# Kernel optimization log

Measured on AMD Instinct MI355X. Metric: run time of the kernel, lower is better.

## Reference

```python
import jax, jax.numpy as jnp
import numpy as np

N_Q, M, D, DV = 4096, 32768, 512, 512  # groups, keys, key dim, value dim


def setup_inputs() -> dict:
    key = jax.random.key(0)
    k1, k2, k3 = jax.random.split(key, 3)
    query = jax.random.normal(k1, (N_Q, D), dtype=jnp.float32)
    keys = jax.random.normal(k2, (M, D), dtype=jnp.float32)
    values = jax.random.normal(k3, (M, DV), dtype=jnp.float32)
    # each query/group owns exactly M//N_Q keys -> no empty softmax rows
    tree_idx = jnp.arange(M, dtype=jnp.int32) % N_Q
    return {"query": query, "keys": keys, "values": values, "tree_idx": tree_idx}


def _l2_normalize(x, eps=1e-12):
    # matches F.normalize(x, dim=1, p=2): x / max(||x||_2, eps)
    n = jnp.linalg.norm(x, axis=1, keepdims=True)
    return x / jnp.maximum(n, eps)


def reference(query, keys, values, tree_idx):
    n_q = query.shape[0]
    # mask[q, m] = (tree_idx[m] == q); equivalent to zeros.index_add(0, tree_idx, eye(M)).bool()
    mask = tree_idx[None, :] == jnp.arange(n_q, dtype=tree_idx.dtype)[:, None]  # [N_q, M]
    query_n = _l2_normalize(query)
    keys_n = _l2_normalize(keys)
    align = query_n @ keys_n.T                      # [N_q, M] cosine similarities
    align = jnp.where(mask, align, -jnp.inf)        # masked_fill_(~mask, -inf)
    alpha = jax.nn.softmax(align, axis=1)           # segment-masked softmax per query
    att = alpha @ values                            # [N_q, DV]
    return att, alpha.sum(axis=0)
```

## Files before the change

kernel.cpp:

```cpp
#include <hip/hip_runtime.h>
#include <math.h>

#define D_DIM 512

__device__ __forceinline__ float d4(const float4& a, const float4& b) {
    return a.x*b.x + a.y*b.y + a.z*b.z + a.w*b.w;
}
__device__ __forceinline__ void fma4(float4& a, float w, const float4& v) {
    a.x += w*v.x; a.y += w*v.y; a.z += w*v.z; a.w += w*v.w;
}

__global__ void k_fill(const int* __restrict__ tree_idx, int m_total, int n_q,
                       int cap, int* __restrict__ cnt, int* __restrict__ keyslot) {
    const int i = blockIdx.x * blockDim.x + threadIdx.x;
    const int base = cnt[n_q];
    if (i < m_total) {
        const int q = tree_idx[i];
        const int old = atomicAdd(&cnt[q], 1);
        const int slot = (int)((unsigned)old - (unsigned)base);
        if (slot >= 0 && slot < cap) keyslot[(size_t)q * cap + slot] = i;
    }
}

__global__ __launch_bounds__(256, 8) void attn_main(
        const float* __restrict__ query, const float* __restrict__ keys,
        const float* __restrict__ values, const int* __restrict__ cnt,
        const int* __restrict__ keyslot, int cap,
        const int* __restrict__ tree_idx, int m_total,
        float* __restrict__ att, float* __restrict__ colsum, int n_q) {
    __shared__ float4 s_acc[2][128];
    __shared__ float  s_ps[2][2];
    const int lane = threadIdx.x & 63;
    const int wv   = threadIdx.x >> 6;
    const int ql   = wv >> 1;
    const int h    = wv & 1;
    const int qi   = (blockIdx.x << 1) + ql;
    const bool act = qi < n_q;

    float e0 = 0.f, e1 = 0.f, e2 = 0.f, e3 = 0.f;
    int   m0 = 0, m1 = 0, m2 = 0, m3 = 0;
    bool  ok0 = false, ok1 = false, ok2 = false, ok3 = false;
    float4 aa = make_float4(0.f, 0.f, 0.f, 0.f);
    float4 ab = make_float4(0.f, 0.f, 0.f, 0.f);
    size_t off = 0;
    int nk = 0;
    bool fast = false;

    if (act) {
        const int base = cnt[n_q];
        nk = (int)((unsigned)cnt[qi] - (unsigned)base);
        if (nk < 0) nk = 0;
        if (nk > cap) nk = cap;
        off  = (size_t)qi * cap;
        fast = (nk == 8);
        const float4* qp = (const float4*)(query + (size_t)qi * D_DIM);
        float4 qa = qp[lane], qb = qp[lane + 64];
        float pq = d4(qa, qa) + d4(qb, qb);
        float psum = 0.f;

        if (fast) {
            m0 = keyslot[off + h];     m1 = keyslot[off + h + 2];
            m2 = keyslot[off + h + 4]; m3 = keyslot[off + h + 6];
            ok0 = (m0 >= 0 && m0 < m_total && tree_idx[m0] == qi);
            ok1 = (m1 >= 0 && m1 < m_total && tree_idx[m1] == qi);
            ok2 = (m2 >= 0 && m2 < m_total && tree_idx[m2] == qi);
            ok3 = (m3 >= 0 && m3 < m_total && tree_idx[m3] == qi);
            int c0 = ok0 ? m0 : 0, c1 = ok1 ? m1 : 0;
            int c2 = ok2 ? m2 : 0, c3 = ok3 ? m3 : 0;
            const float4* k0 = (const float4*)(keys + (size_t)c0 * D_DIM);
            const float4* k1 = (const float4*)(keys + (size_t)c1 * D_DIM);
            const float4* k2 = (const float4*)(keys + (size_t)c2 * D_DIM);
            const float4* k3 = (const float4*)(keys + (size_t)c3 * D_DIM);
            float4 x0a = k0[lane], x0b = k0[lane + 64];
            float4 x1a = k1[lane], x1b = k1[lane + 64];
            float pd0 = d4(qa, x0a) + d4(qb, x0b), pk0 = d4(x0a, x0a) + d4(x0b, x0b);
            float pd1 = d4(qa, x1a) + d4(qb, x1b), pk1 = d4(x1a, x1a) + d4(x1b, x1b);
            float4 x2a = k2[lane], x2b = k2[lane + 64];
            float4 x3a = k3[lane], x3b = k3[lane + 64];
            float pd2 = d4(qa, x2a) + d4(qb, x2b), pk2 = d4(x2a, x2a) + d4(x2b, x2b);
            float pd3 = d4(qa, x3a) + d4(qb, x3b), pk3 = d4(x3a, x3a) + d4(x3b, x3b);
#pragma unroll
            for (int o = 32; o > 0; o >>= 1) {
                pq  += __shfl_xor(pq,  o);
                pd0 += __shfl_xor(pd0, o); pk0 += __shfl_xor(pk0, o);
                pd1 += __shfl_xor(pd1, o); pk1 += __shfl_xor(pk1, o);
                pd2 += __shfl_xor(pd2, o); pk2 += __shfl_xor(pk2, o);
                pd3 += __shfl_xor(pd3, o); pk3 += __shfl_xor(pk3, o);
            }
            const float qinv = 1.0f / fmaxf(sqrtf(pq), 1e-12f);
            e0 = ok0 ? __expf(pd0 * qinv / fmaxf(sqrtf(pk0), 1e-12f)) : 0.f;
            e1 = ok1 ? __expf(pd1 * qinv / fmaxf(sqrtf(pk1), 1e-12f)) : 0.f;
            e2 = ok2 ? __expf(pd2 * qinv / fmaxf(sqrtf(pk2), 1e-12f)) : 0.f;
            e3 = ok3 ? __expf(pd3 * qinv / fmaxf(sqrtf(pk3), 1e-12f)) : 0.f;
            psum = e0 + e1 + e2 + e3;
            if (lane == 0) s_ps[ql][h] = psum;
            const float4* v0 = (const float4*)(values + (size_t)c0 * D_DIM);
            const float4* v1 = (const float4*)(values + (size_t)c1 * D_DIM);
            const float4* v2 = (const float4*)(values + (size_t)c2 * D_DIM);
            const float4* v3 = (const float4*)(values + (size_t)c3 * D_DIM);
            float4 y0a = v0[lane], y0b = v0[lane + 64];
            float4 y1a = v1[lane], y1b = v1[lane + 64];
            fma4(aa, e0, y0a); fma4(ab, e0, y0b);
            fma4(aa, e1, y1a); fma4(ab, e1, y1b);
            float4 y2a = v2[lane], y2b = v2[lane + 64];
            float4 y3a = v3[lane], y3b = v3[lane + 64];
            fma4(aa, e2, y2a); fma4(ab, e2, y2b);
            fma4(aa, e3, y3a); fma4(ab, e3, y3b);
        } else {
#pragma unroll
            for (int o = 32; o > 0; o >>= 1) pq += __shfl_xor(pq, o);
            const float qinv = 1.0f / fmaxf(sqrtf(pq), 1e-12f);
            for (int j = h; j < nk; j += 2) {
                int mi = keyslot[off + j];
                bool ok = (mi >= 0 && mi < m_total && tree_idx[mi] == qi);
                int ci = ok ? mi : 0;
                const float4* kp = (const float4*)(keys   + (size_t)ci * D_DIM);
                const float4* vp = (const float4*)(values + (size_t)ci * D_DIM);
                float4 ka = kp[lane], kb = kp[lane + 64];
                float pd = d4(qa, ka) + d4(qb, kb);
                float pk = d4(ka, ka) + d4(kb, kb);
#pragma unroll
                for (int o = 32; o > 0; o >>= 1) {
                    pd += __shfl_xor(pd, o);
                    pk += __shfl_xor(pk, o);
                }
                float e = ok ? __expf(pd * qinv / fmaxf(sqrtf(pk), 1e-12f)) : 0.f;
                psum += e;
                if (lane == 0 && ok) colsum[mi] = e;
                float4 va = vp[lane], vb = vp[lane + 64];
                fma4(aa, e, va); fma4(ab, e, vb);
            }
            if (lane == 0) s_ps[ql][h] = psum;
        }
        if (h == 0) { s_acc[ql][lane] = aa; s_acc[ql][64 + lane] = ab; }
    }
    __syncthreads();
    if (act) {
        const float tot = s_ps[ql][0] + s_ps[ql][1];
        const float inv = (tot > 0.f) ? 1.0f / tot : 0.f;
        if (h == 1) {
            float4 oa = s_acc[ql][lane], ob = s_acc[ql][64 + lane];
            oa.x = (oa.x + aa.x) * inv; oa.y = (oa.y + aa.y) * inv;
            oa.z = (oa.z + aa.z) * inv; oa.w = (oa.w + aa.w) * inv;
            ob.x = (ob.x + ab.x) * inv; ob.y = (ob.y + ab.y) * inv;
            ob.z = (ob.z + ab.z) * inv; ob.w = (ob.w + ab.w) * inv;
            float4* op = (float4*)(att + (size_t)qi * D_DIM);
            op[lane]      = oa;
            op[lane + 64] = ob;
        }
        if (fast) {
            if (lane == 0) {
                if (ok0) colsum[m0] = e0 * inv;
                if (ok1) colsum[m1] = e1 * inv;
                if (ok2) colsum[m2] = e2 * inv;
                if (ok3) colsum[m3] = e3 * inv;
            }
        } else if (lane == 0) {
            for (int j = h; j < nk; j += 2) {
                int mi = keyslot[off + j];
                if (mi >= 0 && mi < m_total && tree_idx[mi] == qi) colsum[mi] *= inv;
            }
        }
    }
}

__global__ void k_zero(int* cnt, int n) {
    int i = blockIdx.x * blockDim.x + threadIdx.x;
    if (i < n) cnt[i] = 0;
}
__global__ void k_count(const int* __restrict__ t, int* __restrict__ cnt, int m) {
    int i = blockIdx.x * blockDim.x + threadIdx.x;
    if (i < m) atomicAdd(&cnt[t[i]], 1);
}
__global__ __launch_bounds__(1024) void k_scan(int* __restrict__ cnt,
                                               int* __restrict__ offsets, int n_q) {
    __shared__ int wsum[16];
    const int tid = threadIdx.x, lane = tid & 63, wv = tid >> 6;
    const int items = (n_q + 1023) >> 10;
    const int base = tid * items;
    int local = 0;
    for (int i = 0; i < items; ++i) { int idx = base + i; if (idx < n_q) local += cnt[idx]; }
    int incl = local;
#pragma unroll
    for (int o = 1; o < 64; o <<= 1) { int v = __shfl_up(incl, o); if (lane >= o) incl += v; }
    if (lane == 63) wsum[wv] = incl;
    __syncthreads();
    if (wv == 0) {
        int v = (lane < 16) ? wsum[lane] : 0;
        int iv = v;
#pragma unroll
        for (int o = 1; o < 16; o <<= 1) { int t = __shfl_up(iv, o); if (lane >= o) iv += t; }
        if (lane < 16) wsum[lane] = iv - v;
    }
    __syncthreads();
    int run = wsum[wv] + incl - local;
    for (int i = 0; i < items; ++i) {
        int idx = base + i;
        if (idx < n_q) { int c = cnt[idx]; offsets[idx] = run; cnt[idx] = run; run += c; }
    }
    if (tid == 1023) offsets[n_q] = run;
}
__global__ void k_scatter(const int* __restrict__ t, int* __restrict__ cnt,
                          int* __restrict__ keylist, int m) {
    int i = blockIdx.x * blockDim.x + threadIdx.x;
    if (i < m) { int p = atomicAdd(&cnt[t[i]], 1); keylist[p] = i; }
}
__global__ __launch_bounds__(512, 8) void attn_fb(
        const float* __restrict__ query, const float* __restrict__ keys,
        const float* __restrict__ values, const int* __restrict__ offsets,
        const int* __restrict__ keylist, float* __restrict__ att,
        float* __restrict__ colsum) {
    __shared__ float4 s_v[8][128];
    __shared__ float  s_e[8];
    const int qi = blockIdx.x, tid = threadIdx.x, lane = tid & 63, wv = tid >> 6;
    const int off = offsets[qi];
    const int nk  = offsets[qi + 1] - off;
    const float4* qp = (const float4*)(query + (size_t)qi * D_DIM);
    float4 qa = qp[lane], qb = qp[lane + 64];
    float pq = d4(qa, qa) + d4(qb, qb);
    float4 aa = make_float4(0,0,0,0), ab = make_float4(0,0,0,0);
    float esum = 0.f;
    for (int idx = wv; idx < nk; idx += 8) {
        const int mi = keylist[off + idx];
        const float4* kp = (const float4*)(keys   + (size_t)mi * D_DIM);
        const float4* vp = (const float4*)(values + (size_t)mi * D_DIM);
        float4 ka = kp[lane], kb = kp[lane + 64];
        float4 va = vp[lane], vb = vp[lane + 64];
        float pd = d4(qa, ka) + d4(qb, kb);
        float pk = d4(ka, ka) + d4(kb, kb);
        float pq2 = pq;
#pragma unroll
        for (int o = 32; o > 0; o >>= 1) {
            pd += __shfl_xor(pd, o); pk += __shfl_xor(pk, o); pq2 += __shfl_xor(pq2, o);
        }
        const float qinv = 1.0f / fmaxf(sqrtf(pq2), 1e-12f);
        const float e = __expf(pd * qinv / fmaxf(sqrtf(pk), 1e-12f));
        esum += e;
        if (lane == 0) colsum[mi] = e;
        fma4(aa, e, va); fma4(ab, e, vb);
    }
    if (lane == 0) s_e[wv] = esum;
    s_v[wv][lane] = aa; s_v[wv][64 + lane] = ab;
    __syncthreads();
    const float tot = s_e[0]+s_e[1]+s_e[2]+s_e[3]+s_e[4]+s_e[5]+s_e[6]+s_e[7];
    const float inv = (tot > 0.f) ? 1.0f / tot : 0.f;
    if (tid < 128) {
        float4 r = s_v[0][tid];
#pragma unroll
        for (int j = 1; j < 8; ++j) { float4 p = s_v[j][tid]; r.x+=p.x; r.y+=p.y; r.z+=p.z; r.w+=p.w; }
        r.x *= inv; r.y *= inv; r.z *= inv; r.w *= inv;
        ((float4*)(att + (size_t)qi * D_DIM))[tid] = r;
    }
    if (lane == 0)
        for (int idx = wv; idx < nk; idx += 8) colsum[keylist[off + idx]] *= inv;
}

extern "C" void kernel_launch(void* const* d_in, const int* in_sizes, int n_in,
                              void* d_out, int out_size, void* d_ws, size_t ws_size,
                              hipStream_t stream) {
    const float* query    = (const float*)d_in[0];
    const float* keys     = (const float*)d_in[1];
    const float* values   = (const float*)d_in[2];
    const int*   tree_idx = (const int*)d_in[3];

    const int n_q     = in_sizes[0] / D_DIM;
    const int m_total = in_sizes[3];

    float* att    = (float*)d_out;
    float* colsum = att + (size_t)n_q * D_DIM;

    const long ws_ints = (long)(ws_size / 4);
    long cap_l = (ws_ints - (n_q + 1)) / (n_q > 0 ? n_q : 1);
    if (cap_l > 1024) cap_l = 1024;

    if (cap_l >= 8) {
        const int cap = (int)cap_l;
        int* cnt     = (int*)d_ws;
        int* keyslot = cnt + n_q + 1;
        k_fill<<<(m_total + 255) / 256, 256, 0, stream>>>(tree_idx, m_total, n_q,
                                                          cap, cnt, keyslot);
        attn_main<<<(n_q + 1) / 2, 256, 0, stream>>>(query, keys, values, cnt,
                                                     keyslot, cap, tree_idx, m_total,
                                                     att, colsum, n_q);
    } else {
        int* cnt     = (int*)d_ws;
        int* offsets = cnt + n_q;
        int* keylist = offsets + n_q + 1;
        k_zero   <<<(n_q + 255) / 256, 256, 0, stream>>>(cnt, n_q);
        k_count  <<<(m_total + 255) / 256, 256, 0, stream>>>(tree_idx, cnt, m_total);
        k_scan   <<<1, 1024, 0, stream>>>(cnt, offsets, n_q);
        k_scatter<<<(m_total + 255) / 256, 256, 0, stream>>>(tree_idx, cnt, keylist, m_total);
        attn_fb  <<<n_q, 512, 0, stream>>>(query, keys, values, offsets, keylist, att, colsum);
    }
}
```

Before: 167.7 us.

## Stage gathered key/value rows into LDS via global_load_lds, one wave per query

Replaces the 4-wave, 2-queries-per-block kernel with a single-wave kernel that processes several queries in sequence. For groups of exactly eight keys, it copies all key and value rows straight into LDS with async global_load_lds before computing, then reads them back from LDS. The goal is more memory-level parallelism for the gathered loads and no cross-wave reduction. The cost is 32 KB of LDS per 64-thread block, which limits occupancy, and queries within a block now run serially.

Result: no change. 170.3 us (+1.5%).

```diff
diff --git a/kernel.cpp b/kernel.cpp
--- a/kernel.cpp
+++ b/kernel.cpp
@@ -8,6 +8,12 @@
 }
 __device__ __forceinline__ void fma4(float4& a, float w, const float4& v) {
     a.x += w*v.x; a.y += w*v.y; a.z += w*v.z; a.w += w*v.w;
+}
+
+__device__ __forceinline__ void g2l16(const float* g, float* l) {
+    __builtin_amdgcn_global_load_lds(
+        (const __attribute__((address_space(1))) void*)g,
+        (__attribute__((address_space(3))) void*)l, 16, 0, 0);
 }
 
 __global__ void k_fill(const int* __restrict__ tree_idx, int m_total, int n_q,
@@ -22,95 +28,104 @@
     }
 }
 
-__global__ __launch_bounds__(256, 8) void attn_main(
+__global__ __launch_bounds__(64) void attn_staged(
         const float* __restrict__ query, const float* __restrict__ keys,
         const float* __restrict__ values, const int* __restrict__ cnt,
         const int* __restrict__ keyslot, int cap,
         const int* __restrict__ tree_idx, int m_total,
-        float* __restrict__ att, float* __restrict__ colsum, int n_q) {
-    __shared__ float4 s_acc[2][128];
-    __shared__ float  s_ps[2][2];
-    const int lane = threadIdx.x & 63;
-    const int wv   = threadIdx.x >> 6;
-    const int ql   = wv >> 1;
-    const int h    = wv & 1;
-    const int qi   = (blockIdx.x << 1) + ql;
-    const bool act = qi < n_q;
-
-    float e0 = 0.f, e1 = 0.f, e2 = 0.f, e3 = 0.f;
-    int   m0 = 0, m1 = 0, m2 = 0, m3 = 0;
-    bool  ok0 = false, ok1 = false, ok2 = false, ok3 = false;
-    float4 aa = make_float4(0.f, 0.f, 0.f, 0.f);
-    float4 ab = make_float4(0.f, 0.f, 0.f, 0.f);
-    size_t off = 0;
-    int nk = 0;
-    bool fast = false;
-
-    if (act) {
-        const int base = cnt[n_q];
-        nk = (int)((unsigned)cnt[qi] - (unsigned)base);
+        float* __restrict__ att, float* __restrict__ colsum, int n_q, int qpb) {
+    extern __shared__ float smem[];
+    const int lane = threadIdx.x;
+    const int q0   = blockIdx.x * qpb;
+    const int base = cnt[n_q];
+
+    for (int it = 0; it < qpb; ++it) {
+        const int qi = q0 + it;
+        if (qi >= n_q) return;
+        int nk = (int)((unsigned)cnt[qi] - (unsigned)base);
         if (nk < 0) nk = 0;
         if (nk > cap) nk = cap;
-        off  = (size_t)qi * cap;
-        fast = (nk == 8);
+        const size_t off = (size_t)qi * cap;
+
         const float4* qp = (const float4*)(query + (size_t)qi * D_DIM);
         float4 qa = qp[lane], qb = qp[lane + 64];
-        float pq = d4(qa, qa) + d4(qb, qb);
-        float psum = 0.f;
-
-        if (fast) {
-            m0 = keyslot[off + h];     m1 = keyslot[off + h + 2];
-            m2 = keyslot[off + h + 4]; m3 = keyslot[off + h + 6];
-            ok0 = (m0 >= 0 && m0 < m_total && tree_idx[m0] == qi);
-            ok1 = (m1 >= 0 && m1 < m_total && tree_idx[m1] == qi);
-            ok2 = (m2 >= 0 && m2 < m_total && tree_idx[m2] == qi);
-            ok3 = (m3 >= 0 && m3 < m_total && tree_idx[m3] == qi);
-            int c0 = ok0 ? m0 : 0, c1 = ok1 ? m1 : 0;
-            int c2 = ok2 ? m2 : 0, c3 = ok3 ? m3 : 0;
-            const float4* k0 = (const float4*)(keys + (size_t)c0 * D_DIM);
-            const float4* k1 = (const float4*)(keys + (size_t)c1 * D_DIM);
-            const float4* k2 = (const float4*)(keys + (size_t)c2 * D_DIM);
-            const float4* k3 = (const float4*)(keys + (size_t)c3 * D_DIM);
-            float4 x0a = k0[lane], x0b = k0[lane + 64];
-            float4 x1a = k1[lane], x1b = k1[lane + 64];
-            float pd0 = d4(qa, x0a) + d4(qb, x0b), pk0 = d4(x0a, x0a) + d4(x0b, x0b);
-            float pd1 = d4(qa, x1a) + d4(qb, x1b), pk1 = d4(x1a, x1a) + d4(x1b, x1b);
-            float4 x2a = k2[lane], x2b = k2[lane + 64];
-            float4 x3a = k3[lane], x3b = k3[lane + 64];
-            float pd2 = d4(qa, x2a) + d4(qb, x2b), pk2 = d4(x2a, x2a) + d4(x2b, x2b);
-            float pd3 = d4(qa, x3a) + d4(qb, x3b), pk3 = d4(x3a, x3a) + d4(x3b, x3b);
+
+        if (nk == 8) {
+            int mv = (lane < 8) ? keyslot[off + lane] : 0;
+            if (mv < 0 || mv >= m_total) mv = 0;
+            int okv = (lane < 8 && tree_idx[mv] == qi) ? 1 : 0;
+            int ms[8];
+#pragma unroll
+            for (int j = 0; j < 8; ++j) ms[j] = __shfl(mv, j);
+
+#pragma unroll
+            for (int j = 0; j < 8; ++j) {
+                const float* kr = keys   + (size_t)ms[j] * D_DIM;
+                const float* vr = values + (size_t)ms[j] * D_DIM;
+                g2l16(kr +       (lane << 2), smem + j * 512);
+                g2l16(kr + 256 + (lane << 2), smem + j * 512 + 256);
+                g2l16(vr +       (lane << 2), smem + 4096 + j * 512);
+                g2l16(vr + 256 + (lane << 2), smem + 4096 + j * 512 + 256);
+            }
+            __syncthreads();
+
+            float pq = d4(qa, qa) + d4(qb, qb);
+            float pd[8], pk[8];
+#pragma unroll
+            for (int j = 0; j < 8; ++j) {
+                const float4* kr = (const float4*)(smem + j * 512);
+                float4 ka = kr[lane], kb = kr[lane + 64];
+                pd[j] = d4(qa, ka) + d4(qb, kb);
+                pk[j] = d4(ka, ka) + d4(kb, kb);
+            }
 #pragma unroll
             for (int o = 32; o > 0; o >>= 1) {
-                pq  += __shfl_xor(pq,  o);
-                pd0 += __shfl_xor(pd0, o); pk0 += __shfl_xor(pk0, o);
-                pd1 += __shfl_xor(pd1, o); pk1 += __shfl_xor(pk1, o);
-                pd2 += __shfl_xor(pd2, o); pk2 += __shfl_xor(pk2, o);
-                pd3 += __shfl_xor(pd3, o); pk3 += __shfl_xor(pk3, o);
+                pq += __shfl_xor(pq, o);
+#pragma unroll
+                for (int j = 0; j < 8; ++j) {
+                    pd[j] += __shfl_xor(pd[j], o);
+                    pk[j] += __shfl_xor(pk[j], o);
+                }
             }
             const float qinv = 1.0f / fmaxf(sqrtf(pq), 1e-12f);
-            e0 = ok0 ? __expf(pd0 * qinv / fmaxf(sqrtf(pk0), 1e-12f)) : 0.f;
-            e1 = ok1 ? __expf(pd1 * qinv / fmaxf(sqrtf(pk1), 1e-12f)) : 0.f;
-            e2 = ok2 ? __expf(pd2 * qinv / fmaxf(sqrtf(pk2), 1e-12f)) : 0.f;
-            e3 = ok3 ? __expf(pd3 * qinv / fmaxf(sqrtf(pk3), 1e-12f)) : 0.f;
-            psum = e0 + e1 + e2 + e3;
-            if (lane == 0) s_ps[ql][h] = psum;
-            const float4* v0 = (const float4*)(values + (size_t)c0 * D_DIM);
-            const float4* v1 = (const float4*)(values + (size_t)c1 * D_DIM);
-            const float4* v2 = (const float4*)(values + (size_t)c2 * D_DIM);
-            const float4* v3 = (const float4*)(values + (size_t)c3 * D_DIM);
-            float4 y0a = v0[lane], y0b = v0[lane + 64];
-            float4 y1a = v1[lane], y1b = v1[lane + 64];
-            fma4(aa, e0, y0a); fma4(ab, e0, y0b);
-            fma4(aa, e1, y1a); fma4(ab, e1, y1b);
-            float4 y2a = v2[lane], y2b = v2[lane + 64];
-            float4 y3a = v3[lane], y3b = v3[lane + 64];
-            fma4(aa, e2, y2a); fma4(ab, e2, y2b);
-            fma4(aa, e3, y3a); fma4(ab, e3, y3b);
+            float e[8], sum = 0.f;
+            int oks[8];
+#pragma unroll
+            for (int j = 0; j < 8; ++j) {
+                oks[j] = __shfl(okv, j);
+                e[j] = oks[j] ? __expf(pd[j] * qinv / fmaxf(sqrtf(pk[j]), 1e-12f)) : 0.f;
+                sum += e[j];
+            }
+            const float inv = (sum > 0.f) ? 1.0f / sum : 0.f;
+
+            float4 aa = make_float4(0.f, 0.f, 0.f, 0.f);
+            float4 ab = make_float4(0.f, 0.f, 0.f, 0.f);
+#pragma unroll
+            for (int j = 0; j < 8; ++j) {
+                const float4* vr = (const float4*)(smem + 4096 + j * 512);
+                float4 va = vr[lane], vb = vr[lane + 64];
+                fma4(aa, e[j], va); fma4(ab, e[j], vb);
+            }
+            aa.x *= inv; aa.y *= inv; aa.z *= inv; aa.w *= inv;
+            ab.x *= inv; ab.y *= inv; ab.z *= inv; ab.w *= inv;
+            float4* op = (float4*)(att + (size_t)qi * D_DIM);
+            op[lane]      = aa;
+            op[lane + 64] = ab;
+            if (lane == 0) {
+#pragma unroll
+                for (int j = 0; j < 8; ++j)
+                    if (oks[j]) colsum[ms[j]] = e[j] * inv;
+            }
+            __syncthreads();
         } else {
+            float pq = d4(qa, qa) + d4(qb, qb);
 #pragma unroll
             for (int o = 32; o > 0; o >>= 1) pq += __shfl_xor(pq, o);
             const float qinv = 1.0f / fmaxf(sqrtf(pq), 1e-12f);
-            for (int j = h; j < nk; j += 2) {
+            float sum = 0.f;
+            float4 aa = make_float4(0.f, 0.f, 0.f, 0.f);
+            float4 ab = make_float4(0.f, 0.f, 0.f, 0.f);
+            for (int j = 0; j < nk; ++j) {
                 int mi = keyslot[off + j];
                 bool ok = (mi >= 0 && mi < m_total && tree_idx[mi] == qi);
                 int ci = ok ? mi : 0;
@@ -124,41 +139,24 @@
                     pd += __shfl_xor(pd, o);
                     pk += __shfl_xor(pk, o);
                 }
-                float e = ok ? __expf(pd * qinv / fmaxf(sqrtf(pk), 1e-12f)) : 0.f;
-                psum += e;
-                if (lane == 0 && ok) colsum[mi] = e;
+                float ev = ok ? __expf(pd * qinv / fmaxf(sqrtf(pk), 1e-12f)) : 0.f;
+                sum += ev;
+                if (lane == 0 && ok) colsum[mi] = ev;
                 float4 va = vp[lane], vb = vp[lane + 64];
-                fma4(aa, e, va); fma4(ab, e, vb);
-            }
-            if (lane == 0) s_ps[ql][h] = psum;
-        }
-        if (h == 0) { s_acc[ql][lane] = aa; s_acc[ql][64 + lane] = ab; }
-    }
-    __syncthreads();
-    if (act) {
-        const float tot = s_ps[ql][0] + s_ps[ql][1];
-        const float inv = (tot > 0.f) ? 1.0f / tot : 0.f;
-        if (h == 1) {
-            float4 oa = s_acc[ql][lane], ob = s_acc[ql][64 + lane];
-            oa.x = (oa.x + aa.x) * inv; oa.y = (oa.y + aa.y) * inv;
-            oa.z = (oa.z + aa.z) * inv; oa.w = (oa.w + aa.w) * inv;
-            ob.x = (ob.x + ab.x) * inv; ob.y = (ob.y + ab.y) * inv;
-            ob.z = (ob.z + ab.z) * inv; ob.w = (ob.w + ab.w) * inv;
+                fma4(aa, ev, va); fma4(ab, ev, vb);
+            }
+            const float inv = (sum > 0.f) ? 1.0f / sum : 0.f;
+            aa.x *= inv; aa.y *= inv; aa.z *= inv; aa.w *= inv;
+            ab.x *= inv; ab.y *= inv; ab.z *= inv; ab.w *= inv;
             float4* op = (float4*)(att + (size_t)qi * D_DIM);
-            op[lane]      = oa;
-            op[lane + 64] = ob;
-        }
-        if (fast) {
+            op[lane]      = aa;
+            op[lane + 64] = ab;
             if (lane == 0) {
-                if (ok0) colsum[m0] = e0 * inv;
-                if (ok1) colsum[m1] = e1 * inv;
-                if (ok2) colsum[m2] = e2 * inv;
-                if (ok3) colsum[m3] = e3 * inv;
-            }
-        } else if (lane == 0) {
-            for (int j = h; j < nk; j += 2) {
-                int mi = keyslot[off + j];
-                if (mi >= 0 && mi < m_total && tree_idx[mi] == qi) colsum[mi] *= inv;
+                for (int j = 0; j < nk; ++j) {
+                    int mi = keyslot[off + j];
+                    if (mi >= 0 && mi < m_total && tree_idx[mi] == qi)
+                        colsum[mi] *= inv;
+                }
             }
         }
     }
@@ -279,9 +277,12 @@
         int* keyslot = cnt + n_q + 1;
         k_fill<<<(m_total + 255) / 256, 256, 0, stream>>>(tree_idx, m_total, n_q,
                                                           cap, cnt, keyslot);
-        attn_main<<<(n_q + 1) / 2, 256, 0, stream>>>(query, keys, values, cnt,
-                                                     keyslot, cap, tree_idx, m_total,
-                                                     att, colsum, n_q);
+        int qpb = (n_q + 1023) / 1024;
+        if (qpb < 1) qpb = 1;
+        int grid = (n_q + qpb - 1) / qpb;
+        attn_staged<<<grid, 64, 32768, stream>>>(query, keys, values, cnt,
+                                                 keyslot, cap, tree_idx, m_total,
+                                                 att, colsum, n_q, qpb);
     } else {
         int* cnt     = (int*)d_ws;
         int* offsets = cnt + n_q;
```
